# Performance work log

Hardware: AMD Instinct MI355X
Metric: run time of the kernel (lower is better)

## Reference

```python
import jax, jax.numpy as jnp
import numpy as np

INPUT_SIZE = 512
HIDDEN_SIZE = 1024
OUTPUT_SIZE = 512

def _xavier(key, shape):
    fan_out, fan_in = shape
    limit = jnp.sqrt(6.0 / (fan_in + fan_out))
    return jax.random.uniform(key, shape, jnp.float32, -limit, limit)

def setup_inputs() -> dict:
    key = jax.random.key(0)
    ks = jax.random.split(key, 6)
    in_h = INPUT_SIZE + HIDDEN_SIZE
    x = jax.random.normal(ks[0], (128, 256, INPUT_SIZE), jnp.float32)
    return {
        "x": x,
        "W_f": _xavier(ks[1], (HIDDEN_SIZE, in_h)), "b_f": jnp.zeros((HIDDEN_SIZE,), jnp.float32),
        "W_i": _xavier(ks[2], (HIDDEN_SIZE, in_h)), "b_i": jnp.zeros((HIDDEN_SIZE,), jnp.float32),
        "W_c": _xavier(ks[3], (HIDDEN_SIZE, in_h)), "b_c": jnp.zeros((HIDDEN_SIZE,), jnp.float32),
        "W_o": _xavier(ks[4], (HIDDEN_SIZE, in_h)), "b_o": jnp.zeros((HIDDEN_SIZE,), jnp.float32),
        "W_out": _xavier(ks[5], (OUTPUT_SIZE, HIDDEN_SIZE)), "b_out": jnp.zeros((OUTPUT_SIZE,), jnp.float32),
    }

def reference(x, W_f, b_f, W_i, b_i, W_c, b_c, W_o, b_o, W_out, b_out):
    B = x.shape[0]
    H = W_f.shape[0]
    h0 = jnp.zeros((B, H), x.dtype)
    c0 = jnp.zeros((B, H), x.dtype)

    def step(carry, x_t):
        h, c = carry
        combined = jnp.concatenate([x_t, h], axis=1)  # [B, In+H]
        f = jax.nn.sigmoid(combined @ W_f.T + b_f)
        i = jax.nn.sigmoid(combined @ W_i.T + b_i)
        c_tilde = jnp.tanh(combined @ W_c.T + b_c)
        o = jax.nn.sigmoid(combined @ W_o.T + b_o)
        c_new = f * c + i * c_tilde
        h_new = o * jnp.tanh(c_new)
        return (h_new, c_new), h_new

    # scan over time: x transposed to [T, B, In]
    (_, _), hs = jax.lax.scan(step, (h0, c0), jnp.swapaxes(x, 0, 1))
    hs = jnp.swapaxes(hs, 0, 1)  # [B, T, H]
    outputs = jnp.einsum('bth,oh->bto', hs, W_out) + b_out
    return outputs
```

## Files before the change

### kernel.cpp

```cpp
#include <hip/hip_runtime.h>
#include <stdint.h>

#define B_   128
#define T_   256
#define IN_  512
#define H_   1024
#define NG_  4096
#define KC_  1536
#define OUT_ 512
#define NBLK 256
#define NTHR 512

typedef __bf16 bf16x8 __attribute__((ext_vector_type(8)));
typedef float  f32x4  __attribute__((ext_vector_type(4)));
typedef unsigned long long ull;

__device__ __forceinline__ ushort f2bf(float f) {
    union { float f; uint32_t u; } v; v.f = f;
    uint32_t u = v.u;
    return (ushort)((u + 0x7FFFu + ((u >> 16) & 1u)) >> 16);
}

__device__ __forceinline__ f32x4 mfma16(bf16x8 a, bf16x8 b, f32x4 c) {
    return __builtin_amdgcn_mfma_f32_16x16x32_bf16(a, b, c, 0, 0, 0);
}

__device__ __forceinline__ float sigf(float x) {
    return 1.f / (1.f + __expf(-x));
}

__device__ __forceinline__ float tanhf_fast(float x) {
    float e = __expf(2.f * x);
    return 1.f - 2.f / (e + 1.f);
}


__global__ void prep_w(const float* __restrict__ Wf, const float* __restrict__ Wi,
                       const float* __restrict__ Wc, const float* __restrict__ Wo,
                       ushort* __restrict__ Wc2) {
    int col = blockIdx.x;
    int j = col >> 2, g = col & 3;
    const float* W = (g == 0) ? Wf : (g == 1) ? Wi : (g == 2) ? Wc : Wo;
    for (int k = threadIdx.x; k < KC_; k += 256)
        Wc2[((size_t)(k >> 5) * NG_ + col) * 32 + (k & 31)] = f2bf(W[(size_t)j * KC_ + k]);
}

__global__ void prep_bias(const float* __restrict__ bf_, const float* __restrict__ bi_,
                          const float* __restrict__ bc_, const float* __restrict__ bo_,
                          float* __restrict__ bias) {
    int idx = blockIdx.x * 256 + threadIdx.x;
    int j = idx >> 2, g = idx & 3;
    const float* b = (g == 0) ? bf_ : (g == 1) ? bi_ : (g == 2) ? bc_ : bo_;
    bias[idx] = b[j];
}

__global__ void prep_wout(const float* __restrict__ W, ushort* __restrict__ Wb) {
    int row = blockIdx.x;
    for (int k = threadIdx.x; k < H_; k += 256)
        Wb[(size_t)row * H_ + k] = f2bf(W[(size_t)row * H_ + k]);
}

__global__ void prep_x(const float* __restrict__ x, ushort* __restrict__ xT) {
    int bid = blockIdx.x;
    int t = bid >> 7, b = bid & 127;
    const float* src = x  + ((size_t)b * T_ + t) * IN_;
    ushort*      dst = xT + ((size_t)t * B_ + b) * IN_;
    for (int k = threadIdx.x; k < IN_; k += 256) dst[k] = f2bf(src[k]);
}

__global__ void prep_zero(ushort* __restrict__ hs0, unsigned int* __restrict__ flags) {
    int idx = blockIdx.x * 256 + threadIdx.x;
    hs0[idx] = 0;
    if (idx < NBLK) flags[idx] = 0u;
}


__launch_bounds__(NTHR, 2)
__global__ void lstm_persist(const ushort* __restrict__ xT,
                             const ushort* __restrict__ Wc2,
                             const float* __restrict__ bias,
                             ushort* __restrict__ hs,
                             unsigned int* flags)
{
    __shared__ ushort As[32 * 1536];
    __shared__ ushort Ws[8 * 6 * 64 * 8];
    __shared__ float  scr[4][2][16][17];

    const int tid  = threadIdx.x;
    const int lane = tid & 63;
    const int wv   = tid >> 6;
    const int nf   = wv & 3;
    const int kh   = wv >> 2;
    const int bx   = blockIdx.x;
    const int grp  = (bx >> 3) & 3;
    const int sub  = (bx & 7) + 8 * (bx >> 5);
    const int nbase = sub * 64;
    const int rbase = grp * 32;

    const int colg  = nbase + nf * 16 + (lane & 15);
    const int g     = lane & 3;
    const int unitg = colg >> 2;

    const float biasv = bias[colg];
    float creg4[4] = {0.f, 0.f, 0.f, 0.f};

    const int srow = tid >> 4;
    const int sc16 = tid & 15;
    const int arow0 = lane & 15;
    const int arow1 = 16 + (lane & 15);
    const int asw  = lane & 15;

    const ushort* wbase = Wc2 + (size_t)colg * 32 + (lane >> 4) * 8;

#pragma unroll
    for (int c7 = 0; c7 < 6; ++c7) {
        uint4 v = *(const uint4*)(wbase + (size_t)(2 * (8 + c7) + kh) * (NG_ * 32));
        *(uint4*)&Ws[(((wv * 6) + c7) * 64 + lane) * 8] = v;
    }
    {
        const ushort* xT0 = xT + ((size_t)(rbase + srow)) * IN_;
#pragma unroll
        for (int j = 0; j < 4; ++j) {
            const int s = j * 16 + sc16;
            uint4 v = *(const uint4*)(xT0 + s * 8);
            *(uint4*)&As[srow * 1536 + (s ^ (srow & 15)) * 8] = v;
        }
    }
    __syncthreads();

    for (int t = 0; t < T_; ++t) {
        bf16x8 wf[4];
#pragma unroll
        for (int s = 0; s < 4; ++s)
            wf[s] = *(const bf16x8*)(wbase + (size_t)(2 * s + kh) * (NG_ * 32));

        f32x4 acc0 = {0.f,0.f,0.f,0.f}, acc1 = {0.f,0.f,0.f,0.f};
#pragma unroll
        for (int i = 0; i < 8; ++i) {
            const int ks = (2 * i + kh) * 4 + (lane >> 4);
            bf16x8 a0 = *(const bf16x8*)&As[arow0 * 1536 + (ks ^ asw) * 8];
            bf16x8 a1 = *(const bf16x8*)&As[arow1 * 1536 + (ks ^ asw) * 8];
            bf16x8 w = wf[i & 3];
            const int nxt = (i < 4) ? (i + 4) : (i + 10);
            wf[i & 3] = *(const bf16x8*)(wbase + (size_t)(2 * nxt + kh) * (NG_ * 32));
            acc0 = mfma16(a0, w, acc0);
            acc1 = mfma16(a1, w, acc1);
        }

        const int tn = (t + 1 < T_) ? (t + 1) : t;
        const ushort* xTn = xT + ((size_t)tn * B_ + rbase + srow) * IN_;
        uint4 vx[4];
#pragma unroll
        for (int j = 0; j < 4; ++j)
            vx[j] = *(const uint4*)(xTn + (j * 16 + sc16) * 8);

        if (t > 0 && wv == 0) {
            const unsigned int* fp =
                flags + (lane & 7) + 8 * grp + 32 * (lane >> 3);
            while (1) {
                unsigned v = __hip_atomic_load(fp, __ATOMIC_RELAXED,
                                               __HIP_MEMORY_SCOPE_AGENT);
                if (__ballot(v < (unsigned)t) == 0ull) break;
                __builtin_amdgcn_s_sleep(1);
            }
        }
        __syncthreads();

        const ull* hrow = (const ull*)(hs + ((size_t)t * B_ + rbase + srow) * H_);
        ull hv[16];
#pragma unroll
        for (int j = 0; j < 16; ++j)
            hv[j] = __hip_atomic_load(hrow + j * 16 + sc16,
                                      __ATOMIC_RELAXED, __HIP_MEMORY_SCOPE_AGENT);
#pragma unroll
        for (int j = 0; j < 4; ++j) {
            const int s = j * 16 + sc16;
            *(uint4*)&As[srow * 1536 + (s ^ (srow & 15)) * 8] = vx[j];
        }
#pragma unroll
        for (int j = 0; j < 16; ++j) {
            const int u   = j * 16 + sc16;
            const int seg = 64 + (u >> 1);
            *(ull*)&As[srow * 1536 + (seg ^ (srow & 15)) * 8 + (u & 1) * 4] = hv[j];
        }
        __syncthreads();

#pragma unroll
        for (int j = 8; j < 14; ++j) {
            const int ks = (2 * j + kh) * 4 + (lane >> 4);
            bf16x8 a0 = *(const bf16x8*)&As[arow0 * 1536 + (ks ^ asw) * 8];
            bf16x8 a1 = *(const bf16x8*)&As[arow1 * 1536 + (ks ^ asw) * 8];
            bf16x8 w = *(const bf16x8*)&Ws[(((wv * 6) + (j - 8)) * 64 + lane) * 8];
            acc0 = mfma16(a0, w, acc0);
            acc1 = mfma16(a1, w, acc1);
        }
#pragma unroll
        for (int j = 14; j < 24; ++j) {
            const int ks = (2 * j + kh) * 4 + (lane >> 4);
            bf16x8 a0 = *(const bf16x8*)&As[arow0 * 1536 + (ks ^ asw) * 8];
            bf16x8 a1 = *(const bf16x8*)&As[arow1 * 1536 + (ks ^ asw) * 8];
            bf16x8 w = wf[(j - 6) & 3];
            if (j <= 19)
                wf[(j - 6) & 3] =
                    *(const bf16x8*)(wbase + (size_t)(2 * (j + 4) + kh) * (NG_ * 32));
            acc0 = mfma16(a0, w, acc0);
            acc1 = mfma16(a1, w, acc1);
        }

        {
            const f32x4 other = kh ? acc0 : acc1;
#pragma unroll
            for (int q = 0; q < 4; ++q)
                scr[nf][kh ^ 1][(lane >> 4) * 4 + q][lane & 15] = other[q];
        }
        __syncthreads();

        {
            const f32x4 own = kh ? acc1 : acc0;
            unsigned int* hout =
                (unsigned int*)(hs + ((size_t)(t + 1) * B_ + rbase) * H_);
#pragma unroll
            for (int q = 0; q < 4; ++q) {
                const int r16 = (lane >> 4) * 4 + q;
                const int row = kh * 16 + r16;
                float v = own[q] + scr[nf][kh][r16][lane & 15] + biasv;
                float a0 = (g == 2) ? tanhf_fast(v) : sigf(v);
                float a1 = __shfl_xor(a0, 1);
                float a2 = __shfl_xor(a0, 2);
                float a3 = __shfl_xor(a1, 2);
                float vf = (g == 0) ? a0 : (g == 1) ? a1 : (g == 2) ? a2 : a3;
                float vi = (g == 0) ? a1 : (g == 1) ? a0 : (g == 2) ? a3 : a2;
                float vc = (g == 0) ? a2 : (g == 1) ? a3 : (g == 2) ? a0 : a1;
                float vo = (g == 0) ? a3 : (g == 1) ? a2 : (g == 2) ? a1 : a0;
                float cn = vf * creg4[q] + vi * vc;
                creg4[q] = cn;
                unsigned int hu = (unsigned int)f2bf(vo * tanhf_fast(cn));
                unsigned int hp = (unsigned int)__shfl_xor((int)hu, 4);
                if ((lane & 7) == 0)
                    __hip_atomic_store(hout + row * 512 + (unitg >> 1),
                                       hu | (hp << 16),
                                       __ATOMIC_RELAXED, __HIP_MEMORY_SCOPE_AGENT);
            }
        }
        __syncthreads();
        if (tid == 0)
            __hip_atomic_store(flags + bx, (unsigned)(t + 1), __ATOMIC_RELAXED,
                               __HIP_MEMORY_SCOPE_AGENT);
    }
}


__launch_bounds__(256, 2)
__global__ void out_gemm(const ushort* __restrict__ hsflat,
                         const ushort* __restrict__ Wout,
                         const float* __restrict__ bout,
                         float* __restrict__ out)
{
    __shared__ ushort As2[128 * 64];
    __shared__ ushort Bs2[64 * 64];
    const int tid  = threadIdx.x;
    const int lane = tid & 63;
    const int wave = tid >> 6;
    const int wm = (wave >> 1) * 64;
    const int wn = (wave & 1) * 32;
    const int mbase = (blockIdx.x >> 3) * 128;
    const int nbase = (blockIdx.x & 7) * 64;

    f32x4 acc[4][2];
#pragma unroll
    for (int i = 0; i < 4; i++)
#pragma unroll
        for (int j = 0; j < 2; j++) acc[i][j] = (f32x4){0.f, 0.f, 0.f, 0.f};

    for (int kc = 0; kc < H_ / 64; ++kc) {
        const int k0 = kc * 64;
        __syncthreads();
#pragma unroll
        for (int it = 0; it < 4; ++it) {
            int gg = it * 256 + tid;
            int row = gg >> 3;
            int seg = gg & 7;
            uint4 v = *(const uint4*)(hsflat + (size_t)(mbase + row) * H_ + k0 + seg * 8);
            int dstg = seg ^ (row & 7);
            *(uint4*)&As2[row * 64 + dstg * 8] = v;
        }
#pragma unroll
        for (int it = 0; it < 2; ++it) {
            int gg = it * 256 + tid;
            int row = gg >> 3;
            int seg = gg & 7;
            uint4 v = *(const uint4*)(Wout + (size_t)(nbase + row) * H_ + k0 + seg * 8);
            int dstg = seg ^ (row & 7);
            *(uint4*)&Bs2[row * 64 + dstg * 8] = v;
        }
        __syncthreads();
#pragma unroll
        for (int ks = 0; ks < 2; ++ks) {
            const int kg = ks * 4 + (lane >> 4);
            bf16x8 af[4], bfr[2];
#pragma unroll
            for (int mi = 0; mi < 4; ++mi) {
                int row = wm + mi * 16 + (lane & 15);
                int gi = kg ^ (row & 7);
                af[mi] = *(const bf16x8*)&As2[row * 64 + gi * 8];
            }
#pragma unroll
            for (int ni = 0; ni < 2; ++ni) {
                int row = wn + ni * 16 + (lane & 15);
                int gi = kg ^ (row & 7);
                bfr[ni] = *(const bf16x8*)&Bs2[row * 64 + gi * 8];
            }
#pragma unroll
            for (int mi = 0; mi < 4; ++mi)
#pragma unroll
                for (int ni = 0; ni < 2; ++ni)
                    acc[mi][ni] = mfma16(af[mi], bfr[ni], acc[mi][ni]);
        }
    }

#pragma unroll
    for (int mi = 0; mi < 4; ++mi) {
#pragma unroll
        for (int ni = 0; ni < 2; ++ni) {
            int col = nbase + wn + ni * 16 + (lane & 15);
            float bv = bout[col];
#pragma unroll
            for (int q = 0; q < 4; ++q) {
                int rt = mbase + wm + mi * 16 + (lane >> 4) * 4 + q;
                int b = rt & 127, tt = rt >> 7;
                out[((size_t)b * T_ + tt) * OUT_ + col] = acc[mi][ni][q] + bv;
            }
        }
    }
}


extern "C" void kernel_launch(void* const* d_in, const int* in_sizes, int n_in,
                              void* d_out, int out_size, void* d_ws, size_t ws_size,
                              hipStream_t stream)
{
    const float* x    = (const float*)d_in[0];
    const float* Wf   = (const float*)d_in[1];
    const float* bf_  = (const float*)d_in[2];
    const float* Wi   = (const float*)d_in[3];
    const float* bi_  = (const float*)d_in[4];
    const float* Wc   = (const float*)d_in[5];
    const float* bc_  = (const float*)d_in[6];
    const float* Wo   = (const float*)d_in[7];
    const float* bo_  = (const float*)d_in[8];
    const float* Wout = (const float*)d_in[9];
    const float* bout = (const float*)d_in[10];
    float* out = (float*)d_out;

    char* ws = (char*)d_ws;
    size_t off = 0;
    auto alloc = [&](size_t bytes) {
        char* p = ws + off;
        off += (bytes + 255) & ~(size_t)255;
        return p;
    };
    ushort* xT   = (ushort*)alloc((size_t)T_ * B_ * IN_ * 2);
    ushort* Wc2  = (ushort*)alloc((size_t)NG_ * KC_ * 2);
    float*  bias = (float*) alloc((size_t)NG_ * 4);
    ushort* Wob  = (ushort*)alloc((size_t)OUT_ * H_ * 2);
    ushort* hs   = (ushort*)alloc((size_t)(T_ + 1) * B_ * H_ * 2);
    unsigned int* flags = (unsigned int*)alloc((size_t)NBLK * 4);

    hipLaunchKernelGGL(prep_w,    dim3(NG_), dim3(256), 0, stream, Wf, Wi, Wc, Wo, Wc2);
    hipLaunchKernelGGL(prep_bias, dim3(16),  dim3(256), 0, stream, bf_, bi_, bc_, bo_, bias);
    hipLaunchKernelGGL(prep_wout, dim3(OUT_),dim3(256), 0, stream, Wout, Wob);
    hipLaunchKernelGGL(prep_x,    dim3(T_ * B_), dim3(256), 0, stream, x, xT);
    hipLaunchKernelGGL(prep_zero, dim3(512), dim3(256), 0, stream, hs, flags);

    hipLaunchKernelGGL(lstm_persist, dim3(NBLK), dim3(NTHR), 0, stream,
                       xT, Wc2, bias, hs, flags);

    hipLaunchKernelGGL(out_gemm, dim3(2048), dim3(256), 0, stream,
                       hs + (size_t)B_ * H_, Wob, bout, out);
}
```

Baseline: 1.756 ms.

## Replace end-of-step barrier with per-wave flag increments and split h staging

Each wave now signals completion by atomically incrementing its block flag after draining its stores, and the poller waits for 8*t increments. This removes the trailing __syncthreads and the single-thread flag store. The h-state loads become 16-byte plain loads instead of 8-byte atomic loads. The LDS staging is split into two halves with a barrier between them, so the MFMAs on the first half of h can run while the second half is being written. Weight prefetches for the later k-slices are restructured into separate registers. Plain non-atomic loads of h data rely on the flag protocol for visibility, which carries a coherence risk.

```diff
diff --git a/kernel.cpp b/kernel.cpp
--- a/kernel.cpp
+++ b/kernel.cpp
@@ -146,6 +146,8 @@
             acc0 = mfma16(a0, w, acc0);
             acc1 = mfma16(a1, w, acc1);
         }
+        bf16x8 wg0 = *(const bf16x8*)(wbase + (size_t)(2 * 18 + kh) * (NG_ * 32));
+        bf16x8 wg1 = *(const bf16x8*)(wbase + (size_t)(2 * 19 + kh) * (NG_ * 32));
 
         const int tn = (t + 1 < T_) ? (t + 1) : t;
         const ushort* xTn = xT + ((size_t)tn * B_ + rbase + srow) * IN_;
@@ -157,33 +159,38 @@
         if (t > 0 && wv == 0) {
             const unsigned int* fp =
                 flags + (lane & 7) + 8 * grp + 32 * (lane >> 3);
+            const unsigned need = 8u * (unsigned)t;
             while (1) {
                 unsigned v = __hip_atomic_load(fp, __ATOMIC_RELAXED,
                                                __HIP_MEMORY_SCOPE_AGENT);
-                if (__ballot(v < (unsigned)t) == 0ull) break;
+                if (__ballot(v < need) == 0ull) break;
                 __builtin_amdgcn_s_sleep(1);
             }
         }
         __syncthreads();
 
-        const ull* hrow = (const ull*)(hs + ((size_t)t * B_ + rbase + srow) * H_);
-        ull hv[16];
-#pragma unroll
-        for (int j = 0; j < 16; ++j)
-            hv[j] = __hip_atomic_load(hrow + j * 16 + sc16,
-                                      __ATOMIC_RELAXED, __HIP_MEMORY_SCOPE_AGENT);
+        const uint4* hrow =
+            (const uint4*)(hs + ((size_t)t * B_ + rbase + srow) * H_);
+        uint4 hq[8];
+#pragma unroll
+        for (int jb = 0; jb < 8; ++jb)
+            hq[jb] = hrow[jb * 16 + sc16];
 #pragma unroll
         for (int j = 0; j < 4; ++j) {
             const int s = j * 16 + sc16;
             *(uint4*)&As[srow * 1536 + (s ^ (srow & 15)) * 8] = vx[j];
         }
 #pragma unroll
-        for (int j = 0; j < 16; ++j) {
-            const int u   = j * 16 + sc16;
-            const int seg = 64 + (u >> 1);
-            *(ull*)&As[srow * 1536 + (seg ^ (srow & 15)) * 8 + (u & 1) * 4] = hv[j];
-        }
-        __syncthreads();
+        for (int jb = 0; jb < 4; ++jb) {
+            const int seg = 64 + jb * 16 + sc16;
+            *(uint4*)&As[srow * 1536 + (seg ^ (srow & 15)) * 8] = hq[jb];
+        }
+        __syncthreads();
+
+        bf16x8 wh[4];
+#pragma unroll
+        for (int s = 0; s < 4; ++s)
+            wh[s] = *(const bf16x8*)(wbase + (size_t)(2 * (20 + s) + kh) * (NG_ * 32));
 
 #pragma unroll
         for (int j = 8; j < 14; ++j) {
@@ -195,14 +202,28 @@
             acc1 = mfma16(a1, w, acc1);
         }
 #pragma unroll
-        for (int j = 14; j < 24; ++j) {
+        for (int j = 14; j < 16; ++j) {
             const int ks = (2 * j + kh) * 4 + (lane >> 4);
             bf16x8 a0 = *(const bf16x8*)&As[arow0 * 1536 + (ks ^ asw) * 8];
             bf16x8 a1 = *(const bf16x8*)&As[arow1 * 1536 + (ks ^ asw) * 8];
-            bf16x8 w = wf[(j - 6) & 3];
-            if (j <= 19)
-                wf[(j - 6) & 3] =
-                    *(const bf16x8*)(wbase + (size_t)(2 * (j + 4) + kh) * (NG_ * 32));
+            bf16x8 w = wf[j - 14];
+            acc0 = mfma16(a0, w, acc0);
+            acc1 = mfma16(a1, w, acc1);
+        }
+#pragma unroll
+        for (int jb = 4; jb < 8; ++jb) {
+            const int seg = 64 + jb * 16 + sc16;
+            *(uint4*)&As[srow * 1536 + (seg ^ (srow & 15)) * 8] = hq[jb];
+        }
+        __syncthreads();
+
+#pragma unroll
+        for (int j = 16; j < 24; ++j) {
+            const int ks = (2 * j + kh) * 4 + (lane >> 4);
+            bf16x8 a0 = *(const bf16x8*)&As[arow0 * 1536 + (ks ^ asw) * 8];
+            bf16x8 a1 = *(const bf16x8*)&As[arow1 * 1536 + (ks ^ asw) * 8];
+            bf16x8 w = (j == 16) ? wf[2] : (j == 17) ? wf[3]
+                     : (j == 18) ? wg0   : (j == 19) ? wg1 : wh[j - 20];
             acc0 = mfma16(a0, w, acc0);
             acc1 = mfma16(a1, w, acc1);
         }
@@ -242,10 +263,10 @@
                                        __ATOMIC_RELAXED, __HIP_MEMORY_SCOPE_AGENT);
             }
         }
-        __syncthreads();
-        if (tid == 0)
-            __hip_atomic_store(flags + bx, (unsigned)(t + 1), __ATOMIC_RELAXED,
-                               __HIP_MEMORY_SCOPE_AGENT);
+        asm volatile("s_waitcnt vmcnt(0)" ::: "memory");
+        if (lane == 0)
+            (void)__hip_atomic_fetch_add(flags + bx, 1u, __ATOMIC_RELAXED,
+                                         __HIP_MEMORY_SCOPE_AGENT);
     }
 }
 
```

After: 4.984 ms. 2.84x slower.
